# Kernel optimization log

Measured on AMD Instinct MI355X. Metric: run time of the kernel, lower is better.

Reference implementation:

```python
import jax, jax.numpy as jnp
import numpy as np

B, S, D, H = 8, 1024, 256, 8
HD = D // H
EPS = 1e-5
NEG = -1000000000.0


def setup_inputs() -> dict:
    key = jax.random.key(0)
    ks = jax.random.split(key, 12)
    s = 1.0 / np.sqrt(D)
    inp = {
        "q": jax.random.normal(ks[0], (B, S, D), jnp.float32),
        "kv_mask": jax.random.randint(ks[1], (B, S), 0, 2) > 0,
        "attn_bias": jax.random.normal(ks[2], (B, S, S, H), jnp.float32),
        "Wq": jax.random.normal(ks[3], (D, D), jnp.float32) * s,
        "bq": jax.random.normal(ks[4], (D,), jnp.float32) * s,
        "Wk": jax.random.normal(ks[5], (D, D), jnp.float32) * s,
        "bk": jax.random.normal(ks[6], (D,), jnp.float32) * s,
        "Wv": jax.random.normal(ks[7], (D, D), jnp.float32) * s,
        "bv": jax.random.normal(ks[8], (D,), jnp.float32) * s,
        "gamma": jnp.ones((D,), jnp.float32),
        "beta": jnp.zeros((D,), jnp.float32),
        "Wo": jax.random.normal(ks[9], (D, D), jnp.float32) * s,
        "bo": jax.random.normal(ks[10], (D,), jnp.float32) * s,
    }
    return inp


def reference(q, kv_mask, attn_bias, Wq, bq, Wk, bk, Wv, bv, gamma, beta, Wo, bo):
    b, s, d = q.shape
    # merge_masks: q_mask all True -> merged = kv_mask broadcast over query dim
    merged = jnp.broadcast_to(kv_mask[:, None, None, :], (b, 1, s, s))  # [b,1,s,s]
    # additive float mask: (~mask)*-1e9 + bias permuted to [b,h,q,k]
    add_mask = (~merged).astype(q.dtype) * NEG + jnp.transpose(attn_bias, (0, 3, 1, 2))
    # projections (torch Linear: x @ W.T + b)
    qh = (q @ Wq.T + bq).reshape(b, s, H, HD).transpose(0, 2, 1, 3)  # [b,h,s,hd]
    kh = (q @ Wk.T + bk).reshape(b, s, H, HD).transpose(0, 2, 1, 3)
    vh = (q @ Wv.T + bv).reshape(b, s, H, HD).transpose(0, 2, 1, 3)
    scores = jnp.einsum("bhqd,bhkd->bhqk", qh, kh) / np.sqrt(HD) + add_mask
    attn = jax.nn.softmax(scores, axis=-1)
    a = jnp.einsum("bhqk,bhkd->bhqd", attn, vh)  # [b,h,s,hd]
    a = a.transpose(0, 2, 1, 3).reshape(b, s, d)
    # LayerNorm (eps=1e-5)
    mu = a.mean(-1, keepdims=True)
    var = ((a - mu) ** 2).mean(-1, keepdims=True)
    a = (a - mu) / jnp.sqrt(var + EPS) * gamma + beta
    return a @ Wo.T + bo
```

## Files before the change

kernel.cpp:

```cpp
#include <hip/hip_runtime.h>
#include <hip/hip_bf16.h>


static constexpr int SEQ = 1024;
static constexpr float SCL  = 0.17677669529663687f;
static constexpr float NEGV = -1000000000.0f;

typedef __attribute__((ext_vector_type(8))) __bf16 bf8v;
typedef __attribute__((ext_vector_type(4))) float  f4v;

__device__ __forceinline__ f4v mfma16(bf8v a, bf8v b, f4v c) {
  return __builtin_amdgcn_mfma_f32_16x16x32_bf16(a, b, c, 0, 0, 0);
}
__device__ __forceinline__ unsigned short bfbits(float f) {
  __hip_bfloat16 hbf = __float2bfloat16(f);
  unsigned short u; __builtin_memcpy(&u, &hbf, 2); return u;
}
__device__ __forceinline__ float bf2f(unsigned short u) {
  unsigned x = ((unsigned)u) << 16; float f; __builtin_memcpy(&f, &x, 4); return f;
}
__device__ __forceinline__ void lds_barrier() {
  __builtin_amdgcn_sched_barrier(0);
  asm volatile("s_waitcnt lgkmcnt(0)" ::: "memory");
  __builtin_amdgcn_s_barrier();
  __builtin_amdgcn_sched_barrier(0);
}

__global__ __launch_bounds__(256) void prep_kernel(
    const float* __restrict__ q, const float* __restrict__ Wq,
    const float* __restrict__ Wk, const float* __restrict__ Wv,
    const float* __restrict__ Wo, const int* __restrict__ km,
    __hip_bfloat16* __restrict__ q_bf, __hip_bfloat16* __restrict__ w_bf,
    float* __restrict__ mskf)
{
  const int NQ4 = (8192 * 256) / 4;
  const int NW4 = 65536 / 4;
  int t = threadIdx.x;

  if (blockIdx.x == 2304) {
    __shared__ int isbool;
    if (t == 0) isbool = 0;
    __syncthreads();
    const unsigned* u = (const unsigned*)km;
    int any = 0;
    for (int i = t; i < 2048; i += 256)
      if (u[i] & ~1u) any = 1;
    if (any) isbool = 1;
    __syncthreads();
    const unsigned char* b8 = (const unsigned char*)km;
    for (int i = t; i < 8192; i += 256) {
      int mv = isbool ? (int)b8[i] : km[i];
      mskf[i] = mv ? 0.f : NEGV;
    }
    return;
  }

  int i = blockIdx.x * 256 + t;
  const float4* src; __hip_bfloat16* dst;
  if (i < NQ4) {
    src = (const float4*)q + i;
    dst = q_bf + (long)i * 4;
  } else {
    int j = i - NQ4; int w = j >> 14; int o4 = j & (NW4 - 1);
    const float* sp = (w == 0) ? Wq : (w == 1) ? Wk : (w == 2) ? Wv : Wo;
    src = (const float4*)sp + o4;
    dst = w_bf + w * 65536 + o4 * 4;
  }
  float4 v = *src;
  ushort4 pk;
  pk.x = bfbits(v.x); pk.y = bfbits(v.y); pk.z = bfbits(v.z); pk.w = bfbits(v.w);
  *reinterpret_cast<ushort4*>(dst) = pk;
}

__global__ __launch_bounds__(256) void qkv_gemm(
    const __hip_bfloat16* __restrict__ q_bf, const __hip_bfloat16* __restrict__ w_bf,
    const float* __restrict__ bq, const float* __restrict__ bk,
    const float* __restrict__ bv,
    __hip_bfloat16* __restrict__ qh, __hip_bfloat16* __restrict__ kh,
    __hip_bfloat16* __restrict__ vt)
{
  int z = blockIdx.z;
  int w = threadIdx.x >> 6;
  int l = threadIdx.x & 63, lr = l & 15, lg = l >> 4;

  const __hip_bfloat16 *A, *Bm; const float* bias; __hip_bfloat16* out;
  long ldOut; int m0, n0;
  if (z < 2) {
    A = q_bf; Bm = w_bf + z * 65536; bias = z ? bk : bq; out = z ? kh : qh;
    ldOut = 256;
    m0 = blockIdx.x * 64; n0 = blockIdx.y * 128 + w * 32;
  } else {
    A = w_bf + 2 * 65536; Bm = q_bf; bias = bv; out = vt; ldOut = 8192;
    int bid = blockIdx.y * 128 + blockIdx.x;
    m0 = (bid >> 6) * 64; n0 = (bid & 63) * 128 + w * 32;
  }

  f4v acc[4][2];
#pragma unroll
  for (int mt = 0; mt < 4; ++mt)
#pragma unroll
    for (int nt = 0; nt < 2; ++nt) acc[mt][nt] = f4v{0.f, 0.f, 0.f, 0.f};

  const __hip_bfloat16* Ab = A  + (long)(m0 + lr) * 256 + lg * 8;
  const __hip_bfloat16* Bb = Bm + (long)(n0 + lr) * 256 + lg * 8;
#pragma unroll
  for (int k0 = 0; k0 < 256; k0 += 32) {
    bf8v af[4], bfr[2];
#pragma unroll
    for (int mt = 0; mt < 4; ++mt)
      af[mt] = *reinterpret_cast<const bf8v*>(Ab + (long)mt * 16 * 256 + k0);
#pragma unroll
    for (int nt = 0; nt < 2; ++nt)
      bfr[nt] = *reinterpret_cast<const bf8v*>(Bb + (long)nt * 16 * 256 + k0);
#pragma unroll
    for (int mt = 0; mt < 4; ++mt)
#pragma unroll
      for (int nt = 0; nt < 2; ++nt)
        acc[mt][nt] = mfma16(af[mt], bfr[nt], acc[mt][nt]);
  }

#pragma unroll
  for (int mt = 0; mt < 4; ++mt) {
    int mrow = m0 + mt * 16 + lg * 4;
#pragma unroll
    for (int nt = 0; nt < 2; ++nt) {
      int ncol = n0 + nt * 16 + lr;
#pragma unroll
      for (int r = 0; r < 4; ++r) {
        float v = acc[mt][nt][r] + ((z == 2) ? bias[mrow + r] : bias[ncol]);
        if (z == 0) v *= SCL;
        out[(long)(mrow + r) * ldOut + ncol] = __float2bfloat16(v);
      }
    }
  }
}

__global__ __launch_bounds__(512, 2) void attn_kernel(
    const __hip_bfloat16* __restrict__ qh, const __hip_bfloat16* __restrict__ kh,
    const __hip_bfloat16* __restrict__ vt, const float* __restrict__ bias,
    const float* __restrict__ mskf, float* __restrict__ af)
{
  __shared__ __align__(16) char smem[53248];
  __hip_bfloat16* bsm = (__hip_bfloat16*)smem;
  __hip_bfloat16* psm = (__hip_bfloat16*)(smem + 38912);
  float* msk = (float*)(smem + 49152);

  int wg = blockIdx.x;
  int bb = wg & 7;
  int hg = (wg >> 3) & 1;
  int qt = wg >> 4;
  int t = threadIdx.x;
  int wid = t >> 6;
  int hl = wid & 3;
  int wq = wid >> 2;
  int h  = hg * 4 + hl;
  int l  = t & 63, lr = l & 15, lg = l >> 4;
  int q0 = qt * 64;
  long bS = (long)bb * SEQ;
  int sq = t >> 3, kq = t & 7;

  for (int i = t; i < 1024; i += 512) msk[i] = mskf[bS + i];

  bf8v qf[2];
#pragma unroll
  for (int qs = 0; qs < 2; ++qs)
    qf[qs] = *reinterpret_cast<const bf8v*>(
        qh + (bS + q0 + wq * 32 + qs * 16 + lr) * 256 + h * 32 + lg * 8);

  f4v o[2][2];
  float lsum[2] = {0.f, 0.f};
#pragma unroll
  for (int qs = 0; qs < 2; ++qs)
#pragma unroll
    for (int nt = 0; nt < 2; ++nt) o[qs][nt] = f4v{0.f, 0.f, 0.f, 0.f};

  const float* bgb = bias + (bS + q0 + sq) * 8192L + hg * 4;

  auto loadBias = [&](int tile, float4 (&br)[4]) {
    int kb = tile * 32;
#pragma unroll
    for (int kk = 0; kk < 4; ++kk)
      br[kk] = *reinterpret_cast<const float4*>(bgb + (long)(kb + 4 * kq + kk) * 8);
  };
  auto cvtWrite = [&](int buf, const float4 (&br)[4], int tile) {
    int kb = tile * 32;
    float mk[4];
#pragma unroll
    for (int kk = 0; kk < 4; ++kk) mk[kk] = msk[kb + 4 * kq + kk];
    __hip_bfloat16* bp = bsm + buf * 9728 + sq * 152 + 4 * kq;
    float w_[4][4] = {{br[0].x, br[0].y, br[0].z, br[0].w},
                      {br[1].x, br[1].y, br[1].z, br[1].w},
                      {br[2].x, br[2].y, br[2].z, br[2].w},
                      {br[3].x, br[3].y, br[3].z, br[3].w}};
#pragma unroll
    for (int c = 0; c < 4; ++c) {
      ushort4 hb;
      hb.x = bfbits(w_[0][c] + mk[0]); hb.y = bfbits(w_[1][c] + mk[1]);
      hb.z = bfbits(w_[2][c] + mk[2]); hb.w = bfbits(w_[3][c] + mk[3]);
      *reinterpret_cast<ushort4*>(bp + c * 36) = hb;
    }
  };
  auto loadKV = [&](int tile, bf8v (&kf)[2], bf8v (&vf)[2]) {
    int kbase = tile * 32;
#pragma unroll
    for (int nt = 0; nt < 2; ++nt)
      kf[nt] = *reinterpret_cast<const bf8v*>(
          kh + (bS + kbase + nt * 16 + lr) * 256 + h * 32 + lg * 8);
#pragma unroll
    for (int n2 = 0; n2 < 2; ++n2)
      vf[n2] = *reinterpret_cast<const bf8v*>(
          vt + (long)(h * 32 + n2 * 16 + lr) * 8192 + bS + kbase + lg * 8);
  };

  auto compute = [&](int kt, const bf8v (&kf)[2], const bf8v (&vf)[2]) {
    const __hip_bfloat16* bbp = bsm + (kt & 1) * 9728;
#pragma unroll
    for (int qs = 0; qs < 2; ++qs) {
      f4v z4 = f4v{0.f, 0.f, 0.f, 0.f};
      f4v s0 = mfma16(kf[0], qf[qs], z4);
      f4v s1 = mfma16(kf[1], qf[qs], z4);

      const __hip_bfloat16* bp = bbp + (wq * 32 + qs * 16 + lr) * 152 + hl * 36;
      ushort4 b0 = *reinterpret_cast<const ushort4*>(bp + lg * 4);
      ushort4 b1 = *reinterpret_cast<const ushort4*>(bp + 16 + lg * 4);

      float p[8];
      p[0] = __expf(s0[0] + bf2f(b0.x)); p[1] = __expf(s0[1] + bf2f(b0.y));
      p[2] = __expf(s0[2] + bf2f(b0.z)); p[3] = __expf(s0[3] + bf2f(b0.w));
      p[4] = __expf(s1[0] + bf2f(b1.x)); p[5] = __expf(s1[1] + bf2f(b1.y));
      p[6] = __expf(s1[2] + bf2f(b1.z)); p[7] = __expf(s1[3] + bf2f(b1.w));
      lsum[qs] += ((p[0] + p[1]) + (p[2] + p[3])) + ((p[4] + p[5]) + (p[6] + p[7]));

      __hip_bfloat16* pw = psm + wid * 640 + lr * 40;
      ushort4 pk0, pk1;
      pk0.x = bfbits(p[0]); pk0.y = bfbits(p[1]); pk0.z = bfbits(p[2]); pk0.w = bfbits(p[3]);
      pk1.x = bfbits(p[4]); pk1.y = bfbits(p[5]); pk1.z = bfbits(p[6]); pk1.w = bfbits(p[7]);
      *reinterpret_cast<ushort4*>(pw + 4 * lg)      = pk0;
      *reinterpret_cast<ushort4*>(pw + 16 + 4 * lg) = pk1;

      bf8v pa = *reinterpret_cast<const bf8v*>(psm + wid * 640 + lr * 40 + lg * 8);
      o[qs][0] = mfma16(pa, vf[0], o[qs][0]);
      o[qs][1] = mfma16(pa, vf[1], o[qs][1]);
    }
  };

  float4 brA[4], brB[4];
  bf8v kfA[2], vfA[2], kfB[2], vfB[2];

  loadBias(0, brA);
  loadBias(1, brB);
  loadKV(0, kfA, vfA);
  lds_barrier();
  cvtWrite(0, brA, 0);
  lds_barrier();

  for (int m = 0; m < 16; ++m) {
    { int kt = 2 * m;
      if (kt + 2 < 32) loadBias(kt + 2, brA);
      loadKV(kt + 1, kfB, vfB);
      compute(kt, kfA, vfA);
      cvtWrite(1, brB, kt + 1);
      lds_barrier(); }
    { int kt = 2 * m + 1;
      if (kt + 2 < 32) { loadBias(kt + 2, brB); loadKV(kt + 1, kfA, vfA); }
      compute(kt, kfB, vfB);
      if (kt + 1 < 32) cvtWrite(0, brA, kt + 1);
      lds_barrier(); }
  }

  float rinv[2];
#pragma unroll
  for (int qs = 0; qs < 2; ++qs) {
    float s = lsum[qs];
    s += __shfl_xor(s, 16);
    s += __shfl_xor(s, 32);
    rinv[qs] = 1.f / s;
  }
#pragma unroll
  for (int qs = 0; qs < 2; ++qs)
#pragma unroll
    for (int r = 0; r < 4; ++r) {
      float invr = __shfl(rinv[qs], lg * 4 + r);
      long row = bS + q0 + wq * 32 + qs * 16 + lg * 4 + r;
      af[row * 256 + h * 32 + lr]      = o[qs][0][r] * invr;
      af[row * 256 + h * 32 + 16 + lr] = o[qs][1][r] * invr;
    }
}

__global__ __launch_bounds__(256) void ln_kernel(
    const float* __restrict__ a, const float* __restrict__ gamma,
    const float* __restrict__ beta, __hip_bfloat16* __restrict__ an)
{
  int row = blockIdx.x * 4 + (threadIdx.x >> 6);
  int l = threadIdx.x & 63;
  const float4 v = *reinterpret_cast<const float4*>(a + (long)row * 256 + l * 4);
  float sm = v.x + v.y + v.z + v.w;
  float sq = v.x * v.x + v.y * v.y + v.z * v.z + v.w * v.w;
#pragma unroll
  for (int m = 1; m < 64; m <<= 1) { sm += __shfl_xor(sm, m); sq += __shfl_xor(sq, m); }
  float mean = sm * (1.f / 256.f);
  float var  = sq * (1.f / 256.f) - mean * mean;
  float rstd = rsqrtf(var + 1e-5f);
  float4 g  = *reinterpret_cast<const float4*>(gamma + l * 4);
  float4 bt = *reinterpret_cast<const float4*>(beta  + l * 4);
  ushort4 pk;
  pk.x = bfbits((v.x - mean) * rstd * g.x + bt.x);
  pk.y = bfbits((v.y - mean) * rstd * g.y + bt.y);
  pk.z = bfbits((v.z - mean) * rstd * g.z + bt.z);
  pk.w = bfbits((v.w - mean) * rstd * g.w + bt.w);
  *reinterpret_cast<ushort4*>(an + (long)row * 256 + l * 4) = pk;
}

__global__ __launch_bounds__(256) void out_proj(
    const __hip_bfloat16* __restrict__ an, const __hip_bfloat16* __restrict__ wob,
    const float* __restrict__ bo, float* __restrict__ outp)
{
  int m0 = blockIdx.x * 64;
  int w  = threadIdx.x >> 6;
  int n0 = blockIdx.y * 128 + w * 32;
  int l  = threadIdx.x & 63, lr = l & 15, lg = l >> 4;

  f4v acc[4][2];
#pragma unroll
  for (int mt = 0; mt < 4; ++mt)
#pragma unroll
    for (int nt = 0; nt < 2; ++nt) acc[mt][nt] = f4v{0.f, 0.f, 0.f, 0.f};

  const __hip_bfloat16* Ab = an  + (long)(m0 + lr) * 256 + lg * 8;
  const __hip_bfloat16* Bb = wob + (long)(n0 + lr) * 256 + lg * 8;
#pragma unroll
  for (int k0 = 0; k0 < 256; k0 += 32) {
    bf8v afr[4], bfr[2];
#pragma unroll
    for (int mt = 0; mt < 4; ++mt)
      afr[mt] = *reinterpret_cast<const bf8v*>(Ab + (long)mt * 16 * 256 + k0);
#pragma unroll
    for (int nt = 0; nt < 2; ++nt)
      bfr[nt] = *reinterpret_cast<const bf8v*>(Bb + (long)nt * 16 * 256 + k0);
#pragma unroll
    for (int mt = 0; mt < 4; ++mt)
#pragma unroll
      for (int nt = 0; nt < 2; ++nt)
        acc[mt][nt] = mfma16(afr[mt], bfr[nt], acc[mt][nt]);
  }

#pragma unroll
  for (int mt = 0; mt < 4; ++mt) {
    int mrow = m0 + mt * 16 + lg * 4;
#pragma unroll
    for (int nt = 0; nt < 2; ++nt) {
      int ncol = n0 + nt * 16 + lr;
      float bov = bo[ncol];
#pragma unroll
      for (int r = 0; r < 4; ++r)
        outp[(long)(mrow + r) * 256 + ncol] = acc[mt][nt][r] + bov;
    }
  }
}

extern "C" void kernel_launch(void* const* d_in, const int* in_sizes, int n_in,
                              void* d_out, int out_size, void* d_ws, size_t ws_size,
                              hipStream_t stream) {
  const float* q   = (const float*)d_in[0];
  const int*   km  = (const int*)d_in[1];
  const float* bias = (const float*)d_in[2];
  const float* Wq = (const float*)d_in[3];
  const float* bq = (const float*)d_in[4];
  const float* Wk = (const float*)d_in[5];
  const float* bk = (const float*)d_in[6];
  const float* Wv = (const float*)d_in[7];
  const float* bv = (const float*)d_in[8];
  const float* gamma = (const float*)d_in[9];
  const float* beta  = (const float*)d_in[10];
  const float* Wo = (const float*)d_in[11];
  const float* bo = (const float*)d_in[12];

  char* wsb = (char*)d_ws;
  __hip_bfloat16* q_bf = (__hip_bfloat16*)(wsb + 0);
  __hip_bfloat16* qh   = (__hip_bfloat16*)(wsb + (4  << 20));
  __hip_bfloat16* kh   = (__hip_bfloat16*)(wsb + (8  << 20));
  __hip_bfloat16* vt   = (__hip_bfloat16*)(wsb + (12 << 20));
  __hip_bfloat16* wbf  = (__hip_bfloat16*)(wsb + (16 << 20));
  float*          mskf = (float*)         (wsb + (17 << 20));
  float*          af   = (float*)         (wsb + (20 << 20));
  __hip_bfloat16* an   = (__hip_bfloat16*)(wsb + (28 << 20));
  __hip_bfloat16* wob  = wbf + 196608;

  prep_kernel<<<2305, 256, 0, stream>>>(q, Wq, Wk, Wv, Wo, km, q_bf, wbf, mskf);
  qkv_gemm<<<dim3(128, 2, 3), 256, 0, stream>>>(q_bf, wbf, bq, bk, bv, qh, kh, vt);
  attn_kernel<<<256, 512, 0, stream>>>(qh, kh, vt, bias, mskf, af);
  ln_kernel<<<2048, 256, 0, stream>>>(af, gamma, beta, an);
  out_proj<<<dim3(128, 2), 256, 0, stream>>>(an, wob, bo, (float*)d_out);
}
```

Before: 140.0 us.

## Split attention over key halves and combine partial sums in layernorm kernel

The attention kernel now assigns each workgroup all 8 heads for 64 queries over one half of the keys (split-K), instead of 4 heads over all keys. Each bias row load then covers all 8 heads contiguously (32 bytes per key), which gives fuller use of each fetched segment of the large bias tensor. Unnormalized partial outputs and row sums are written per half, and a new combine+LayerNorm kernel adds them and normalizes. Without a running max this relies on the exp values not overflowing. It also doubles the af traffic and raises LDS use to about 85KB, which may limit occupancy to one block per CU.

```diff
diff --git a/kernel.cpp b/kernel.cpp
--- a/kernel.cpp
+++ b/kernel.cpp
@@ -138,70 +138,76 @@
 __global__ __launch_bounds__(512, 2) void attn_kernel(
     const __hip_bfloat16* __restrict__ qh, const __hip_bfloat16* __restrict__ kh,
     const __hip_bfloat16* __restrict__ vt, const float* __restrict__ bias,
-    const float* __restrict__ mskf, float* __restrict__ af)
+    const float* __restrict__ mskf, float* __restrict__ af,
+    float* __restrict__ lsums)
 {
-  __shared__ __align__(16) char smem[53248];
+  __shared__ __align__(16) char smem[87040];
   __hip_bfloat16* bsm = (__hip_bfloat16*)smem;
-  __hip_bfloat16* psm = (__hip_bfloat16*)(smem + 38912);
-  float* msk = (float*)(smem + 49152);
+  __hip_bfloat16* psm = (__hip_bfloat16*)(smem + 74752);
+  float* msk = (float*)(smem + 84992);
 
   int wg = blockIdx.x;
-  int bb = wg & 7;
-  int hg = (wg >> 3) & 1;
-  int qt = wg >> 4;
+  int bb  = wg & 7;
+  int khf = (wg >> 3) & 1;
+  int qt  = wg >> 4;
   int t = threadIdx.x;
-  int wid = t >> 6;
-  int hl = wid & 3;
-  int wq = wid >> 2;
-  int h  = hg * 4 + hl;
+  int h  = t >> 6;
   int l  = t & 63, lr = l & 15, lg = l >> 4;
   int q0 = qt * 64;
+  int kOff = khf * 512;
   long bS = (long)bb * SEQ;
   int sq = t >> 3, kq = t & 7;
 
-  for (int i = t; i < 1024; i += 512) msk[i] = mskf[bS + i];
-
-  bf8v qf[2];
-#pragma unroll
-  for (int qs = 0; qs < 2; ++qs)
+  for (int i = t; i < 512; i += 512) msk[i] = mskf[bS + kOff + i];
+
+  bf8v qf[4];
+#pragma unroll
+  for (int qs = 0; qs < 4; ++qs)
     qf[qs] = *reinterpret_cast<const bf8v*>(
-        qh + (bS + q0 + wq * 32 + qs * 16 + lr) * 256 + h * 32 + lg * 8);
-
-  f4v o[2][2];
-  float lsum[2] = {0.f, 0.f};
-#pragma unroll
-  for (int qs = 0; qs < 2; ++qs)
+        qh + (bS + q0 + qs * 16 + lr) * 256 + h * 32 + lg * 8);
+
+  f4v o[4][2];
+  float lsum[4] = {0.f, 0.f, 0.f, 0.f};
+#pragma unroll
+  for (int qs = 0; qs < 4; ++qs)
 #pragma unroll
     for (int nt = 0; nt < 2; ++nt) o[qs][nt] = f4v{0.f, 0.f, 0.f, 0.f};
 
-  const float* bgb = bias + (bS + q0 + sq) * 8192L + hg * 4;
-
-  auto loadBias = [&](int tile, float4 (&br)[4]) {
-    int kb = tile * 32;
-#pragma unroll
-    for (int kk = 0; kk < 4; ++kk)
-      br[kk] = *reinterpret_cast<const float4*>(bgb + (long)(kb + 4 * kq + kk) * 8);
+  const float* bgb = bias + (bS + q0 + sq) * 8192L;
+
+  auto loadBias = [&](int tile, float4 (&br)[8]) {
+    int kb = kOff + tile * 32 + 4 * kq;
+#pragma unroll
+    for (int kk = 0; kk < 4; ++kk) {
+      br[kk * 2]     = *reinterpret_cast<const float4*>(bgb + (long)(kb + kk) * 8);
+      br[kk * 2 + 1] = *reinterpret_cast<const float4*>(bgb + (long)(kb + kk) * 8 + 4);
+    }
   };
-  auto cvtWrite = [&](int buf, const float4 (&br)[4], int tile) {
-    int kb = tile * 32;
+  auto cvtWrite = [&](int buf, const float4 (&br)[8], int tile) {
+    int kl = tile * 32 + 4 * kq;
     float mk[4];
 #pragma unroll
-    for (int kk = 0; kk < 4; ++kk) mk[kk] = msk[kb + 4 * kq + kk];
-    __hip_bfloat16* bp = bsm + buf * 9728 + sq * 152 + 4 * kq;
-    float w_[4][4] = {{br[0].x, br[0].y, br[0].z, br[0].w},
-                      {br[1].x, br[1].y, br[1].z, br[1].w},
-                      {br[2].x, br[2].y, br[2].z, br[2].w},
-                      {br[3].x, br[3].y, br[3].z, br[3].w}};
-#pragma unroll
-    for (int c = 0; c < 4; ++c) {
+    for (int kk = 0; kk < 4; ++kk) mk[kk] = msk[kl + kk];
+    __hip_bfloat16* bp = bsm + buf * 18688 + sq * 292 + 4 * kq;
+#pragma unroll
+    for (int hh = 0; hh < 8; ++hh) {
+      int half = hh >> 2, c = hh & 3;
+      float v0 = (c == 0) ? br[0 + half].x : (c == 1) ? br[0 + half].y
+               : (c == 2) ? br[0 + half].z : br[0 + half].w;
+      float v1 = (c == 0) ? br[2 + half].x : (c == 1) ? br[2 + half].y
+               : (c == 2) ? br[2 + half].z : br[2 + half].w;
+      float v2 = (c == 0) ? br[4 + half].x : (c == 1) ? br[4 + half].y
+               : (c == 2) ? br[4 + half].z : br[4 + half].w;
+      float v3 = (c == 0) ? br[6 + half].x : (c == 1) ? br[6 + half].y
+               : (c == 2) ? br[6 + half].z : br[6 + half].w;
       ushort4 hb;
-      hb.x = bfbits(w_[0][c] + mk[0]); hb.y = bfbits(w_[1][c] + mk[1]);
-      hb.z = bfbits(w_[2][c] + mk[2]); hb.w = bfbits(w_[3][c] + mk[3]);
-      *reinterpret_cast<ushort4*>(bp + c * 36) = hb;
+      hb.x = bfbits(v0 + mk[0]); hb.y = bfbits(v1 + mk[1]);
+      hb.z = bfbits(v2 + mk[2]); hb.w = bfbits(v3 + mk[3]);
+      *reinterpret_cast<ushort4*>(bp + hh * 36) = hb;
     }
   };
   auto loadKV = [&](int tile, bf8v (&kf)[2], bf8v (&vf)[2]) {
-    int kbase = tile * 32;
+    int kbase = kOff + tile * 32;
 #pragma unroll
     for (int nt = 0; nt < 2; ++nt)
       kf[nt] = *reinterpret_cast<const bf8v*>(
@@ -213,14 +219,14 @@
   };
 
   auto compute = [&](int kt, const bf8v (&kf)[2], const bf8v (&vf)[2]) {
-    const __hip_bfloat16* bbp = bsm + (kt & 1) * 9728;
-#pragma unroll
-    for (int qs = 0; qs < 2; ++qs) {
+    const __hip_bfloat16* bbp = bsm + (kt & 1) * 18688;
+#pragma unroll
+    for (int qs = 0; qs < 4; ++qs) {
       f4v z4 = f4v{0.f, 0.f, 0.f, 0.f};
       f4v s0 = mfma16(kf[0], qf[qs], z4);
       f4v s1 = mfma16(kf[1], qf[qs], z4);
 
-      const __hip_bfloat16* bp = bbp + (wq * 32 + qs * 16 + lr) * 152 + hl * 36;
+      const __hip_bfloat16* bp = bbp + (qs * 16 + lr) * 292 + h * 36;
       ushort4 b0 = *reinterpret_cast<const ushort4*>(bp + lg * 4);
       ushort4 b1 = *reinterpret_cast<const ushort4*>(bp + 16 + lg * 4);
 
@@ -231,20 +237,20 @@
       p[6] = __expf(s1[2] + bf2f(b1.z)); p[7] = __expf(s1[3] + bf2f(b1.w));
       lsum[qs] += ((p[0] + p[1]) + (p[2] + p[3])) + ((p[4] + p[5]) + (p[6] + p[7]));
 
-      __hip_bfloat16* pw = psm + wid * 640 + lr * 40;
+      __hip_bfloat16* pw = psm + h * 640 + lr * 40;
       ushort4 pk0, pk1;
       pk0.x = bfbits(p[0]); pk0.y = bfbits(p[1]); pk0.z = bfbits(p[2]); pk0.w = bfbits(p[3]);
       pk1.x = bfbits(p[4]); pk1.y = bfbits(p[5]); pk1.z = bfbits(p[6]); pk1.w = bfbits(p[7]);
       *reinterpret_cast<ushort4*>(pw + 4 * lg)      = pk0;
       *reinterpret_cast<ushort4*>(pw + 16 + 4 * lg) = pk1;
 
-      bf8v pa = *reinterpret_cast<const bf8v*>(psm + wid * 640 + lr * 40 + lg * 8);
+      bf8v pa = *reinterpret_cast<const bf8v*>(psm + h * 640 + lr * 40 + lg * 8);
       o[qs][0] = mfma16(pa, vf[0], o[qs][0]);
       o[qs][1] = mfma16(pa, vf[1], o[qs][1]);
     }
   };
 
-  float4 brA[4], brB[4];
+  float4 brA[8], brB[8];
   bf8v kfA[2], vfA[2], kfB[2], vfB[2];
 
   loadBias(0, brA);
@@ -254,46 +260,52 @@
   cvtWrite(0, brA, 0);
   lds_barrier();
 
-  for (int m = 0; m < 16; ++m) {
+  for (int m = 0; m < 8; ++m) {
     { int kt = 2 * m;
-      if (kt + 2 < 32) loadBias(kt + 2, brA);
+      if (kt + 2 < 16) loadBias(kt + 2, brA);
       loadKV(kt + 1, kfB, vfB);
       compute(kt, kfA, vfA);
       cvtWrite(1, brB, kt + 1);
       lds_barrier(); }
     { int kt = 2 * m + 1;
-      if (kt + 2 < 32) { loadBias(kt + 2, brB); loadKV(kt + 1, kfA, vfA); }
+      if (kt + 2 < 16) { loadBias(kt + 2, brB); loadKV(kt + 1, kfA, vfA); }
       compute(kt, kfB, vfB);
-      if (kt + 1 < 32) cvtWrite(0, brA, kt + 1);
+      if (kt + 1 < 16) cvtWrite(0, brA, kt + 1);
       lds_barrier(); }
   }
 
-  float rinv[2];
-#pragma unroll
-  for (int qs = 0; qs < 2; ++qs) {
+  float* afp = af + (long)khf * 8192 * 256;
+  float* lsp = lsums + (long)khf * 8192 * 8;
+#pragma unroll
+  for (int qs = 0; qs < 4; ++qs) {
     float s = lsum[qs];
     s += __shfl_xor(s, 16);
     s += __shfl_xor(s, 32);
-    rinv[qs] = 1.f / s;
-  }
-#pragma unroll
-  for (int qs = 0; qs < 2; ++qs)
+    if (lg == 0)
+      lsp[(bS + q0 + qs * 16 + lr) * 8 + h] = s;
 #pragma unroll
     for (int r = 0; r < 4; ++r) {
-      float invr = __shfl(rinv[qs], lg * 4 + r);
-      long row = bS + q0 + wq * 32 + qs * 16 + lg * 4 + r;
-      af[row * 256 + h * 32 + lr]      = o[qs][0][r] * invr;
-      af[row * 256 + h * 32 + 16 + lr] = o[qs][1][r] * invr;
-    }
-}
-
-__global__ __launch_bounds__(256) void ln_kernel(
-    const float* __restrict__ a, const float* __restrict__ gamma,
-    const float* __restrict__ beta, __hip_bfloat16* __restrict__ an)
+      long row = bS + q0 + qs * 16 + lg * 4 + r;
+      afp[row * 256 + h * 32 + lr]      = o[qs][0][r];
+      afp[row * 256 + h * 32 + 16 + lr] = o[qs][1][r];
+    }
+  }
+}
+
+__global__ __launch_bounds__(256) void combine_ln_kernel(
+    const float* __restrict__ af, const float* __restrict__ lsums,
+    const float* __restrict__ gamma, const float* __restrict__ beta,
+    __hip_bfloat16* __restrict__ an)
 {
   int row = blockIdx.x * 4 + (threadIdx.x >> 6);
   int l = threadIdx.x & 63;
-  const float4 v = *reinterpret_cast<const float4*>(a + (long)row * 256 + l * 4);
+  int hh = l >> 3;
+  const float4 a0 = *reinterpret_cast<const float4*>(af + (long)row * 256 + l * 4);
+  const float4 a1 = *reinterpret_cast<const float4*>(af + (long)(8192 + row) * 256 + l * 4);
+  float li = 1.f / (lsums[(long)row * 8 + hh] + lsums[(long)(8192 + row) * 8 + hh]);
+  float4 v;
+  v.x = (a0.x + a1.x) * li; v.y = (a0.y + a1.y) * li;
+  v.z = (a0.z + a1.z) * li; v.w = (a0.w + a1.w) * li;
   float sm = v.x + v.y + v.z + v.w;
   float sq = v.x * v.x + v.y * v.y + v.z * v.z + v.w * v.w;
 #pragma unroll
@@ -376,19 +388,20 @@
   const float* bo = (const float*)d_in[12];
 
   char* wsb = (char*)d_ws;
-  __hip_bfloat16* q_bf = (__hip_bfloat16*)(wsb + 0);
-  __hip_bfloat16* qh   = (__hip_bfloat16*)(wsb + (4  << 20));
-  __hip_bfloat16* kh   = (__hip_bfloat16*)(wsb + (8  << 20));
-  __hip_bfloat16* vt   = (__hip_bfloat16*)(wsb + (12 << 20));
-  __hip_bfloat16* wbf  = (__hip_bfloat16*)(wsb + (16 << 20));
-  float*          mskf = (float*)         (wsb + (17 << 20));
-  float*          af   = (float*)         (wsb + (20 << 20));
-  __hip_bfloat16* an   = (__hip_bfloat16*)(wsb + (28 << 20));
-  __hip_bfloat16* wob  = wbf + 196608;
+  __hip_bfloat16* q_bf  = (__hip_bfloat16*)(wsb + 0);
+  __hip_bfloat16* qh    = (__hip_bfloat16*)(wsb + (4  << 20));
+  __hip_bfloat16* kh    = (__hip_bfloat16*)(wsb + (8  << 20));
+  __hip_bfloat16* vt    = (__hip_bfloat16*)(wsb + (12 << 20));
+  __hip_bfloat16* wbf   = (__hip_bfloat16*)(wsb + (16 << 20));
+  float*          mskf  = (float*)         (wsb + (17 << 20));
+  float*          af    = (float*)         (wsb + (20 << 20));
+  float*          lsums = (float*)         (wsb + (36 << 20));
+  __hip_bfloat16* an    = (__hip_bfloat16*)(wsb + (37 << 20));
+  __hip_bfloat16* wob   = wbf + 196608;
 
   prep_kernel<<<2305, 256, 0, stream>>>(q, Wq, Wk, Wv, Wo, km, q_bf, wbf, mskf);
   qkv_gemm<<<dim3(128, 2, 3), 256, 0, stream>>>(q_bf, wbf, bq, bk, bv, qh, kh, vt);
-  attn_kernel<<<256, 512, 0, stream>>>(qh, kh, vt, bias, mskf, af);
-  ln_kernel<<<2048, 256, 0, stream>>>(af, gamma, beta, an);
+  attn_kernel<<<256, 512, 0, stream>>>(qh, kh, vt, bias, mskf, af, lsums);
+  combine_ln_kernel<<<2048, 256, 0, stream>>>(af, lsums, gamma, beta, an);
   out_proj<<<dim3(128, 2), 256, 0, stream>>>(an, wob, bo, (float*)d_out);
 }
```

After: 136.0 us. 1.03x faster.
